# Kernel tuning notes

Hardware: AMD Instinct MI355X
Metric: run time of the kernel (lower is better)

Reference implementation:

```python
import jax, jax.numpy as jnp
import numpy as np

A = 32           # num_atoms
R = A * (A - 1)  # num_rel (fully connected, no self loops)
B, T, D = 4, 64, 64
S, E = 4, 4      # num_states, edge_types
MH, MO, NH = 256, 256, 256

def _lrelu(x):
    return jax.nn.leaky_relu(x, 0.01)  # torch default slope

def setup_inputs() -> dict:
    key = jax.random.key(0)
    ks = jax.random.split(key, 16)
    # one-hot receiver/sender matrices for a fully connected graph
    off = np.ones((A, A)) - np.eye(A)
    rec_idx, send_idx = np.where(off)
    eye = np.eye(A, dtype=np.float32)
    rel_rec = jnp.asarray(eye[rec_idx])    # [R, A]
    rel_send = jnp.asarray(eye[send_idx])  # [R, A]
    w = 0.05
    return {
        "inputs": jax.random.normal(ks[0], (B, A, T, D), jnp.float32),
        "state": jax.random.uniform(ks[1], (B, A, T, S), jnp.float32),
        "rel_type": jax.random.uniform(ks[2], (B, R, S, E), jnp.float32),
        "rel_rec": rel_rec,
        "rel_send": rel_send,
        "msg_fc1_w": jax.random.normal(ks[3], (E, 2 * D, MH), jnp.float32) * w,
        "msg_fc1_b": jax.random.normal(ks[4], (E, MH), jnp.float32) * w,
        "msg_fc2_w": jax.random.normal(ks[5], (E, MH, MO), jnp.float32) * w,
        "msg_fc2_b": jax.random.normal(ks[6], (E, MO), jnp.float32) * w,
        "out_fc1_w": jax.random.normal(ks[7], (D + MO, NH), jnp.float32) * w,
        "out_fc1_b": jax.random.normal(ks[8], (NH,), jnp.float32) * w,
        "out_fc2_w": jax.random.normal(ks[9], (NH, NH), jnp.float32) * w,
        "out_fc2_b": jax.random.normal(ks[10], (NH,), jnp.float32) * w,
        "out_fc3_w": jax.random.normal(ks[11], (NH, D), jnp.float32) * w,
        "out_fc3_b": jax.random.normal(ks[12], (D,), jnp.float32) * w,
        "pred_steps": 1,
    }

def reference(inputs, state, rel_type, rel_rec, rel_send,
              msg_fc1_w, msg_fc1_b, msg_fc2_w, msg_fc2_b,
              out_fc1_w, out_fc1_b, out_fc2_w, out_fc2_b,
              out_fc3_w, out_fc3_b, pred_steps):
    # hidden_states=True, embedding=False, ball_pos=None, skip_first=True,
    # dropout p=0, pred_steps=1 -> one single_step_forward over all T.
    x = jnp.transpose(inputs, (0, 2, 1, 3))   # [B,T,A,D]
    st = jnp.transpose(state, (0, 2, 1, 3))   # [B,T,A,S]
    t = x.shape[1]

    # gather via one-hot matmuls
    recv = jnp.einsum('ra,btad->btrd', rel_rec, x)    # [B,T,R,D]
    send = jnp.einsum('ra,btad->btrd', rel_send, x)   # [B,T,R,D]
    ss = jnp.einsum('ra,btas->btrs', rel_send, st)    # [B,T,R,S]
    pre_msg = jnp.concatenate([send, recv], axis=-1)  # [B,T,R,2D]

    all_msgs = jnp.zeros(pre_msg.shape[:3] + (MO,), pre_msg.dtype)
    for i in range(1, E):  # skip_first_edge_type
        m = _lrelu(pre_msg @ msg_fc1_w[i] + msg_fc1_b[i])
        m = _lrelu(m @ msg_fc2_w[i] + msg_fc2_b[i])
        # gate: sum over states of rel_type[...,i] * sender states
        g = jnp.einsum('brs,btrs->btr', rel_type[..., i], ss)[..., None]
        all_msgs = all_msgs + m * g

    # scatter-accumulate messages back to receiver nodes
    agg = jnp.einsum('btrm,ra->btam', all_msgs, rel_rec)  # [B,T,A,MO]
    aug = jnp.concatenate([x, agg], axis=-1)              # skip_connection = inputs
    h = _lrelu(aug @ out_fc1_w + out_fc1_b)
    h = _lrelu(h @ out_fc2_w + out_fc2_b)
    pred = h @ out_fc3_w + out_fc3_b
    nxt = x + pred                                        # [B,T,A,D]

    out = nxt[:, : t - 1]                                 # pred_all
    return jnp.transpose(out, (0, 2, 1, 3))               # [B,A,T-1,D]
```

## Files before the change

### kernel.cpp

```cpp
#include <hip/hip_runtime.h>


typedef _Float16 f16x8 __attribute__((ext_vector_type(8)));
typedef float f32x4 __attribute__((ext_vector_type(4)));

#define MFMAH(a, b, c) __builtin_amdgcn_mfma_f32_16x16x32_f16((a), (b), (c), 0, 0, 0)

#define KBAR0() do {                                             \
  __builtin_amdgcn_sched_barrier(0);                             \
  asm volatile("s_waitcnt vmcnt(0) lgkmcnt(0)" ::: "memory");    \
  __builtin_amdgcn_s_barrier();                                  \
  __builtin_amdgcn_sched_barrier(0);                             \
} while (0)

__device__ __forceinline__ unsigned pkh(float lo, float hi) {
  auto h = __builtin_amdgcn_cvt_pkrtz(lo, hi);
  return __builtin_bit_cast(unsigned, h);
}
__device__ __forceinline__ unsigned short f2h(float f) {
  return __builtin_bit_cast(unsigned short, (_Float16)f);
}
__device__ __forceinline__ float lrelu(float x) { return x > 0.f ? x : 0.01f * x; }

__device__ __forceinline__ void gl16(const void* g, void* l) {
  __builtin_amdgcn_global_load_lds(
      (const __attribute__((address_space(1))) unsigned int*)(unsigned long long)g,
      (__attribute__((address_space(3))) unsigned int*)(unsigned int)(unsigned long long)l,
      16, 0, 0);
}

__global__ __launch_bounds__(256) void kw(
    const float* __restrict__ w1, const float* __restrict__ w2,
    const float* __restrict__ o1, const float* __restrict__ o2, const float* __restrict__ o3,
    unsigned short* __restrict__ W1T, unsigned short* __restrict__ W2F,
    unsigned short* __restrict__ O1T, unsigned short* __restrict__ O2T,
    unsigned short* __restrict__ O3T) {
  int i = blockIdx.x * 256 + threadIdx.x;
  if (i < 98304) {
    int k = i & 63, n = (i >> 6) & 255, eh = i >> 14;
    int e = (eh >> 1) + 1, half = eh & 1;
    W1T[i] = f2h(w1[(e * 128 + half * 64 + k) * 256 + n]);
    return;
  }
  i -= 98304;
  if (i < 196608) {
    int j = i & 7, l = (i >> 3) & 63, t = (i >> 9) & 15, s = (i >> 13) & 7, e = i >> 16;
    int n = t * 16 + (l & 15);
    int k = s * 32 + (l >> 4) * 8 + j;
    W2F[i] = f2h(w2[(e + 1) * 65536 + k * 256 + n]);
    return;
  }
  i -= 196608;
  if (i < 81920) {
    int k = i % 320, n = i / 320;
    O1T[i] = f2h(o1[k * 256 + n]);
    return;
  }
  i -= 81920;
  if (i < 65536) {
    int k = i & 255, n = i >> 8;
    O2T[i] = f2h(o2[k * 256 + n]);
    return;
  }
  i -= 65536;
  {
    int k = i & 255, n = i >> 8;
    O3T[i] = f2h(o3[k * 64 + n]);
  }
}

__global__ __launch_bounds__(256) void ka(
    const float* __restrict__ inputs, const float* __restrict__ state,
    const float* __restrict__ rel_type, const unsigned short* __restrict__ W1T,
    const float* __restrict__ b1g,
    unsigned short* __restrict__ P, float* __restrict__ G) {
  int t = blockIdx.x, b = blockIdx.y;
  int bt = b * 63 + t;
  int tid = threadIdx.x, lane = tid & 63, wid = tid >> 6;
  int waveM = wid & 1, waveN = wid >> 1;
  __shared__ __align__(16) _Float16 xa[32 * 72];
  __shared__ __align__(16) _Float16 Bt[256 * 72];
  __shared__ __align__(16) _Float16 Ps[32 * 256];
  __shared__ float ss[32][4];
  {
    int a = tid >> 3, d0 = (tid & 7) * 8;
    const float* src = inputs + (((b * 32 + a) * 64 + t) << 6) + d0;
    float4 v0 = *(const float4*)src;
    float4 v1 = *(const float4*)(src + 4);
    uint4 w;
    w.x = pkh(v0.x, v0.y); w.y = pkh(v0.z, v0.w);
    w.z = pkh(v1.x, v1.y); w.w = pkh(v1.z, v1.w);
    *(uint4*)&xa[a * 72 + d0] = w;
  }
  if (tid < 128) {
    int a = tid >> 2, s = tid & 3;
    ss[a][s] = state[((b * 32 + a) * 64 + t) * 4 + s];
  }
  __syncthreads();
  #pragma unroll
  for (int q = 0; q < 12; ++q) {
    int task = tid + q * 256;
    int e = task >> 10, rem = task & 1023, a = rem >> 5, k = rem & 31;
    float g = 0.f;
    if (k < 31) {
      int sA = k + (k >= a ? 1 : 0);
      int r = a * 31 + k;
      const float* rt = rel_type + (b * 992 + r) * 16 + (e + 1);
      g = rt[0] * ss[sA][0] + rt[4] * ss[sA][1] + rt[8] * ss[sA][2] + rt[12] * ss[sA][3];
    }
    G[(bt * 3 + e) * 1024 + a * 32 + k] = g;
  }
  for (int eh = 0; eh < 6; ++eh) {
    #pragma unroll
    for (int q = 0; q < 8; ++q) {
      int cid = tid + q * 256;
      int n = cid >> 3, c8 = (cid & 7) * 8;
      *(uint4*)&Bt[n * 72 + c8] = *(const uint4*)&W1T[(eh * 256 + n) * 64 + c8];
    }
    __syncthreads();
    f32x4 acc[8];
    #pragma unroll
    for (int f = 0; f < 8; ++f) acc[f] = f32x4{0.f, 0.f, 0.f, 0.f};
    #pragma unroll
    for (int ik = 0; ik < 2; ++ik) {
      int k0 = ik * 32;
      f16x8 av = *(const f16x8*)&xa[(waveM * 16 + (lane & 15)) * 72 + k0 + (lane >> 4) * 8];
      #pragma unroll
      for (int f = 0; f < 8; ++f) {
        f16x8 bv = *(const f16x8*)&Bt[(waveN * 128 + f * 16 + (lane & 15)) * 72 + k0 + (lane >> 4) * 8];
        acc[f] = MFMAH(av, bv, acc[f]);
      }
    }
    #pragma unroll
    for (int f = 0; f < 8; ++f) {
      int c = waveN * 128 + f * 16 + (lane & 15);
      float bias = (eh & 1) ? b1g[((eh >> 1) + 1) * 256 + c] : 0.f;
      #pragma unroll
      for (int i = 0; i < 4; ++i) {
        int rrow = waveM * 16 + (lane >> 4) * 4 + i;
        Ps[rrow * 256 + c] = (_Float16)(acc[f][i] + bias);
      }
    }
    __syncthreads();
    unsigned short* dst = P + (bt * 6 + eh) * 8192;
    #pragma unroll
    for (int q = 0; q < 4; ++q) {
      int o = (tid + q * 256) * 8;
      *(uint4*)&dst[o] = *(const uint4*)&Ps[o];
    }
    __syncthreads();
  }
}

__global__ __launch_bounds__(512, 6) void kb(
    const unsigned short* __restrict__ P, const float* __restrict__ G,
    const unsigned short* __restrict__ W2F, const float* __restrict__ b2g,
    unsigned short* __restrict__ AGG3) {
  int bx = blockIdx.x;
  int swz = (bx & 7) * 1512 + (bx >> 3);
  int e = swz / 4032;
  int rem = swz - e * 4032;
  int bt = rem >> 4;
  int sub = rem & 15;
  int q = sub >> 1, nh = sub & 1;
  int a0 = q * 4;
  int tid = threadIdx.x, lane = tid & 63, wid = tid >> 6;
  int waveM = wid & 3, waveN = wid >> 2;
  int lane15 = lane & 15, kqh = lane >> 4;

  __shared__ __align__(16) _Float16 h1F[2][4096];
  __shared__ __align__(16) _Float16 Bt[3][4096];
  __shared__ float gs[128];
  __shared__ float b2s[128];

  const unsigned short* psrc  = P + (bt * 6 + e * 2) * 8192;
  const unsigned short* prsrc = psrc + 8192;
  const unsigned short* w2f = W2F + e * 65536 + nh * 8 * 512;

  int rrow = wid * 16 + lane15;
  int al0 = rrow >> 5, bk = rrow & 31;
  int bs = (bk < 31) ? bk + (bk >= a0 + al0 ? 1 : 0) : 0;
  const unsigned short* pvg = psrc + bs * 256 + kqh * 8;
  const unsigned short* rvg = prsrc + (a0 + al0) * 256 + kqh * 8;
  int h1off = wid * 512 + lane * 8;

  {
    f16x8 pv0 = *(const f16x8*)(pvg);
    f16x8 rv0 = *(const f16x8*)(rvg);
    __builtin_amdgcn_sched_barrier(0);
    gl16(w2f + tid * 8, (char*)&Bt[0][0] + tid * 16);
    gl16(w2f + 8192 + tid * 8, (char*)&Bt[1][0] + tid * 16);
    if (tid < 128) gs[tid] = G[((bt * 3 + e) << 10) + a0 * 32 + tid];
    else if (tid < 256) b2s[tid - 128] = b2g[(e + 1) * 256 + nh * 128 + (tid - 128)];
    f16x8 h = pv0 + rv0;
    *(f16x8*)&h1F[0][h1off] = __builtin_elementwise_max(h, h * (_Float16)0.01f);
  }
  KBAR0();

  f32x4 acc[2][4];
  #pragma unroll
  for (int f = 0; f < 2; ++f)
    #pragma unroll
    for (int g2 = 0; g2 < 4; ++g2) acc[f][g2] = f32x4{0.f, 0.f, 0.f, 0.f};

  #pragma unroll
  for (int s = 0; s < 8; ++s) {
    const int buf = s & 1;
    f16x8 pv, rv;
    if (s < 7) {
      pv = *(const f16x8*)(pvg + (s + 1) * 32);
      rv = *(const f16x8*)(rvg + (s + 1) * 32);
    }
    __builtin_amdgcn_sched_barrier(0);
    if (s < 6)
      gl16(w2f + (s + 2) * 8192 + tid * 8, (char*)&Bt[(s + 2) % 3][0] + tid * 16);
    __builtin_amdgcn_sched_barrier(0);
    f16x8 af0 = *(const f16x8*)&h1F[buf][(waveM * 2 + 0) * 512 + lane * 8];
    f16x8 af1 = *(const f16x8*)&h1F[buf][(waveM * 2 + 1) * 512 + lane * 8];
    __builtin_amdgcn_s_setprio(1);
    #pragma unroll
    for (int g2 = 0; g2 < 4; ++g2) {
      f16x8 bv = *(const f16x8*)&Bt[s % 3][(waveN * 4 + g2) * 512 + lane * 8];
      acc[0][g2] = MFMAH(af0, bv, acc[0][g2]);
      acc[1][g2] = MFMAH(af1, bv, acc[1][g2]);
    }
    __builtin_amdgcn_s_setprio(0);
    if (s < 7) {
      f16x8 h = pv + rv;
      *(f16x8*)&h1F[buf ^ 1][h1off] = __builtin_elementwise_max(h, h * (_Float16)0.01f);
      __builtin_amdgcn_sched_barrier(0);
      if (s < 6) asm volatile("s_waitcnt vmcnt(1)" ::: "memory");
      else       asm volatile("s_waitcnt vmcnt(0)" ::: "memory");
      asm volatile("s_waitcnt lgkmcnt(0)" ::: "memory");
      __builtin_amdgcn_s_barrier();
      __builtin_amdgcn_sched_barrier(0);
    }
  }

  _Float16* aggh = (_Float16*)AGG3;
  int al = a0 + waveM;
  #pragma unroll
  for (int g2 = 0; g2 < 4; ++g2) {
    int cl = (waveN * 4 + g2) * 16 + lane15;
    float bb = b2s[cl];
    float p = 0.f;
    #pragma unroll
    for (int f = 0; f < 2; ++f) {
      int k4 = f * 16 + kqh * 4;
      #pragma unroll
      for (int i = 0; i < 4; ++i)
        p += gs[waveM * 32 + k4 + i] * lrelu(acc[f][g2][i] + bb);
    }
    p += __shfl_xor(p, 16, 64);
    p += __shfl_xor(p, 32, 64);
    if (lane < 16)
      aggh[(size_t)e * 2064384 + (((bt * 32 + al) << 8) + nh * 128 + cl)] = (_Float16)p;
  }
}

__global__ __launch_bounds__(256) void kc(
    const float* __restrict__ inputs, const unsigned short* __restrict__ AGG3,
    const unsigned short* __restrict__ O1T, const unsigned short* __restrict__ O2T,
    const unsigned short* __restrict__ O3T,
    const float* __restrict__ ob1, const float* __restrict__ ob2, const float* __restrict__ ob3,
    float* __restrict__ out) {
  int t = blockIdx.x, b = blockIdx.y;
  int bt = b * 63 + t;
  int tid = threadIdx.x, lane = tid & 63, wid = tid >> 6;
  int waveM = wid & 1, waveN = wid >> 1;
  __shared__ __align__(16) _Float16 aug[32 * 328];
  __shared__ __align__(16) _Float16 h1[32 * 264];
  __shared__ __align__(16) _Float16 h2[32 * 264];
  __shared__ __align__(16) _Float16 Bt[256 * 40];
  __shared__ __align__(16) float xs[32 * 64];
  __shared__ float lb1[256], lb2[256], lb3[64];
  {
    int a = tid >> 3, d0 = (tid & 7) * 8;
    const float* src = inputs + (((b * 32 + a) * 64 + t) << 6) + d0;
    float4 v0 = *(const float4*)src;
    float4 v1 = *(const float4*)(src + 4);
    *(float4*)&xs[a * 64 + d0] = v0;
    *(float4*)&xs[a * 64 + d0 + 4] = v1;
    uint4 w;
    w.x = pkh(v0.x, v0.y); w.y = pkh(v0.z, v0.w);
    w.z = pkh(v1.x, v1.y); w.w = pkh(v1.z, v1.w);
    *(uint4*)&aug[a * 328 + d0] = w;
  }
  #pragma unroll
  for (int qq = 0; qq < 4; ++qq) {
    int cid = tid + qq * 256;
    int a = cid >> 5, c8 = (cid & 31) * 8;
    size_t o = ((size_t)(bt * 32 + a) << 8) + c8;
    f16x8 v0 = *(const f16x8*)&AGG3[o];
    f16x8 v1 = *(const f16x8*)&AGG3[2064384 + o];
    f16x8 v2 = *(const f16x8*)&AGG3[4128768 + o];
    f16x8 s = v0 + v1 + v2;
    *(uint4*)&aug[a * 328 + 64 + c8] = __builtin_bit_cast(uint4, s);
  }
  lb1[tid] = ob1[tid];
  lb2[tid] = ob2[tid];
  if (tid < 64) lb3[tid] = ob3[tid];
  __syncthreads();
  f32x4 acc[8];
  #pragma unroll
  for (int f = 0; f < 8; ++f) acc[f] = f32x4{0.f, 0.f, 0.f, 0.f};
  for (int kk = 0; kk < 10; ++kk) {
    #pragma unroll
    for (int q = 0; q < 4; ++q) {
      int cid = tid + q * 256;
      int n = cid >> 2, c8 = (cid & 3) * 8;
      *(uint4*)&Bt[n * 40 + c8] = *(const uint4*)&O1T[n * 320 + kk * 32 + c8];
    }
    __syncthreads();
    f16x8 av = *(const f16x8*)&aug[(waveM * 16 + (lane & 15)) * 328 + kk * 32 + (lane >> 4) * 8];
    #pragma unroll
    for (int f = 0; f < 8; ++f) {
      f16x8 bv = *(const f16x8*)&Bt[(waveN * 128 + f * 16 + (lane & 15)) * 40 + (lane >> 4) * 8];
      acc[f] = MFMAH(av, bv, acc[f]);
    }
    __syncthreads();
  }
  #pragma unroll
  for (int f = 0; f < 8; ++f) {
    int c = waveN * 128 + f * 16 + (lane & 15);
    #pragma unroll
    for (int i = 0; i < 4; ++i) {
      int r = waveM * 16 + (lane >> 4) * 4 + i;
      h1[r * 264 + c] = (_Float16)lrelu(acc[f][i] + lb1[c]);
    }
  }
  __syncthreads();
  #pragma unroll
  for (int f = 0; f < 8; ++f) acc[f] = f32x4{0.f, 0.f, 0.f, 0.f};
  for (int kk = 0; kk < 8; ++kk) {
    #pragma unroll
    for (int q = 0; q < 4; ++q) {
      int cid = tid + q * 256;
      int n = cid >> 2, c8 = (cid & 3) * 8;
      *(uint4*)&Bt[n * 40 + c8] = *(const uint4*)&O2T[n * 256 + kk * 32 + c8];
    }
    __syncthreads();
    f16x8 av = *(const f16x8*)&h1[(waveM * 16 + (lane & 15)) * 264 + kk * 32 + (lane >> 4) * 8];
    #pragma unroll
    for (int f = 0; f < 8; ++f) {
      f16x8 bv = *(const f16x8*)&Bt[(waveN * 128 + f * 16 + (lane & 15)) * 40 + (lane >> 4) * 8];
      acc[f] = MFMAH(av, bv, acc[f]);
    }
    __syncthreads();
  }
  #pragma unroll
  for (int f = 0; f < 8; ++f) {
    int c = waveN * 128 + f * 16 + (lane & 15);
    #pragma unroll
    for (int i = 0; i < 4; ++i) {
      int r = waveM * 16 + (lane >> 4) * 4 + i;
      h2[r * 264 + c] = (_Float16)lrelu(acc[f][i] + lb2[c]);
    }
  }
  __syncthreads();
  f32x4 a3[2];
  a3[0] = f32x4{0.f, 0.f, 0.f, 0.f};
  a3[1] = f32x4{0.f, 0.f, 0.f, 0.f};
  for (int kk = 0; kk < 8; ++kk) {
    {
      int n = tid >> 2, c8 = (tid & 3) * 8;
      *(uint4*)&Bt[n * 40 + c8] = *(const uint4*)&O3T[n * 256 + kk * 32 + c8];
    }
    __syncthreads();
    f16x8 av = *(const f16x8*)&h2[(waveM * 16 + (lane & 15)) * 264 + kk * 32 + (lane >> 4) * 8];
    #pragma unroll
    for (int f = 0; f < 2; ++f) {
      f16x8 bv = *(const f16x8*)&Bt[(waveN * 32 + f * 16 + (lane & 15)) * 40 + (lane >> 4) * 8];
      a3[f] = MFMAH(av, bv, a3[f]);
    }
    __syncthreads();
  }
  #pragma unroll
  for (int f = 0; f < 2; ++f) {
    int d = waveN * 32 + f * 16 + (lane & 15);
    #pragma unroll
    for (int i = 0; i < 4; ++i) {
      int a = waveM * 16 + (lane >> 4) * 4 + i;
      out[((b * 32 + a) * 63 + t) * 64 + d] = a3[f][i] + lb3[d] + xs[a * 64 + d];
    }
  }
}

extern "C" void kernel_launch(void* const* d_in, const int* in_sizes, int n_in,
                              void* d_out, int out_size, void* d_ws, size_t ws_size,
                              hipStream_t stream) {
  const float* inputs   = (const float*)d_in[0];
  const float* state    = (const float*)d_in[1];
  const float* rel_type = (const float*)d_in[2];
  const float* w1  = (const float*)d_in[5];
  const float* b1  = (const float*)d_in[6];
  const float* w2  = (const float*)d_in[7];
  const float* b2  = (const float*)d_in[8];
  const float* o1w = (const float*)d_in[9];
  const float* o1b = (const float*)d_in[10];
  const float* o2w = (const float*)d_in[11];
  const float* o2b = (const float*)d_in[12];
  const float* o3w = (const float*)d_in[13];
  const float* o3b = (const float*)d_in[14];
  char* ws = (char*)d_ws;
  unsigned short* W1T = (unsigned short*)(ws + 0);
  unsigned short* W2F = (unsigned short*)(ws + 196608);
  unsigned short* O1T = (unsigned short*)(ws + 589824);
  unsigned short* O2T = (unsigned short*)(ws + 753664);
  unsigned short* O3T = (unsigned short*)(ws + 884736);
  unsigned short* Pp  = (unsigned short*)(ws + 917504);
  float* G    = (float*)(ws + 25690112);
  unsigned short* AGG3 = (unsigned short*)(ws + 28786688);
  float* out = (float*)d_out;

  kw<<<1792, 256, 0, stream>>>(w1, w2, o1w, o2w, o3w, W1T, W2F, O1T, O2T, O3T);
  ka<<<dim3(63, 4), 256, 0, stream>>>(inputs, state, rel_type, W1T, b1, Pp, G);
  kb<<<12096, 512, 0, stream>>>(Pp, G, W2F, b2, AGG3);
  kc<<<dim3(63, 4), 256, 0, stream>>>(inputs, AGG3, O1T, O2T, O3T, o1b, o2b, o3b, out);
}
```

Measured before the change: 191.8 us.

## Preload whole weight slice into LDS and build A fragments in registers

Kernel kb now loads the entire 64KB W2 slice for its N-half into shared memory up front, instead of streaming it through a triple-buffered ring. Each wave builds its own A-operand fragments (leaky-relu of P+R) directly in registers rather than writing h1 to LDS and reading it back. This removes the per-step block barriers and LDS round trips. In exchange, LDS use grows from about 40KB to 64KB per block, so the occupancy hint drops from 6 to 4, which reduces latency hiding. All weight loads also now sit before the first compute.

Measured after the change: 269.0 us. 40.3% more time.

```diff
diff --git a/kernel.cpp b/kernel.cpp
--- a/kernel.cpp
+++ b/kernel.cpp
@@ -152,7 +152,7 @@
   }
 }
 
-__global__ __launch_bounds__(512, 6) void kb(
+__global__ __launch_bounds__(512, 4) void kb(
     const unsigned short* __restrict__ P, const float* __restrict__ G,
     const unsigned short* __restrict__ W2F, const float* __restrict__ b2g,
     unsigned short* __restrict__ AGG3) {
@@ -168,77 +168,78 @@
   int waveM = wid & 3, waveN = wid >> 2;
   int lane15 = lane & 15, kqh = lane >> 4;
 
-  __shared__ __align__(16) _Float16 h1F[2][4096];
-  __shared__ __align__(16) _Float16 Bt[3][4096];
+  __shared__ __align__(16) _Float16 Bp[32768];
   __shared__ float gs[128];
   __shared__ float b2s[128];
 
   const unsigned short* psrc  = P + (bt * 6 + e * 2) * 8192;
   const unsigned short* prsrc = psrc + 8192;
-  const unsigned short* w2f = W2F + e * 65536 + nh * 8 * 512;
-
-  int rrow = wid * 16 + lane15;
-  int al0 = rrow >> 5, bk = rrow & 31;
-  int bs = (bk < 31) ? bk + (bk >= a0 + al0 ? 1 : 0) : 0;
-  const unsigned short* pvg = psrc + bs * 256 + kqh * 8;
-  const unsigned short* rvg = prsrc + (a0 + al0) * 256 + kqh * 8;
-  int h1off = wid * 512 + lane * 8;
-
+  const unsigned short* w2f   = W2F + e * 65536 + nh * 4096;
+
+  int al = a0 + waveM;
+  int bk0 = lane15;
+  int bk1 = 16 + lane15;
+  int bs0 = bk0 + (bk0 >= al ? 1 : 0);
+  int bs1 = (bk1 < 31) ? (bk1 + (bk1 >= al ? 1 : 0)) : 0;
+  const unsigned short* pv0g = psrc + bs0 * 256 + kqh * 8;
+  const unsigned short* pv1g = psrc + bs1 * 256 + kqh * 8;
+  const unsigned short* rvg  = prsrc + al * 256 + kqh * 8;
+
+  f16x8 pvA = *(const f16x8*)pv0g;
+  f16x8 pvB = *(const f16x8*)pv1g;
+  f16x8 rv0 = *(const f16x8*)rvg;
+  __builtin_amdgcn_sched_barrier(0);
+  #pragma unroll
+  for (int j = 0; j < 8; ++j) {
+    int c = j * 512 + tid;
+    gl16(w2f + (c >> 9) * 8192 + (c & 511) * 8, (char*)&Bp[0] + c * 16);
+  }
+  if (tid < 128) gs[tid] = G[((bt * 3 + e) << 10) + a0 * 32 + tid];
+  else if (tid < 256) b2s[tid - 128] = b2g[(e + 1) * 256 + nh * 128 + (tid - 128)];
+  f16x8 af0, af1;
   {
-    f16x8 pv0 = *(const f16x8*)(pvg);
-    f16x8 rv0 = *(const f16x8*)(rvg);
+    f16x8 h = pvA + rv0;
+    af0 = __builtin_elementwise_max(h, h * (_Float16)0.01f);
+    h = pvB + rv0;
+    af1 = __builtin_elementwise_max(h, h * (_Float16)0.01f);
+  }
+  KBAR0();
+
+  f32x4 acc[2][4];
+  #pragma unroll
+  for (int f = 0; f < 2; ++f)
+    #pragma unroll
+    for (int g2 = 0; g2 < 4; ++g2) acc[f][g2] = f32x4{0.f, 0.f, 0.f, 0.f};
+
+  #pragma unroll
+  for (int s = 0; s < 8; ++s) {
+    f16x8 pA, pB, rN;
+    if (s < 7) {
+      pA = *(const f16x8*)(pv0g + (s + 1) * 32);
+      pB = *(const f16x8*)(pv1g + (s + 1) * 32);
+      rN = *(const f16x8*)(rvg + (s + 1) * 32);
+    }
     __builtin_amdgcn_sched_barrier(0);
-    gl16(w2f + tid * 8, (char*)&Bt[0][0] + tid * 16);
-    gl16(w2f + 8192 + tid * 8, (char*)&Bt[1][0] + tid * 16);
-    if (tid < 128) gs[tid] = G[((bt * 3 + e) << 10) + a0 * 32 + tid];
-    else if (tid < 256) b2s[tid - 128] = b2g[(e + 1) * 256 + nh * 128 + (tid - 128)];
-    f16x8 h = pv0 + rv0;
-    *(f16x8*)&h1F[0][h1off] = __builtin_elementwise_max(h, h * (_Float16)0.01f);
-  }
-  KBAR0();
-
-  f32x4 acc[2][4];
-  #pragma unroll
-  for (int f = 0; f < 2; ++f)
-    #pragma unroll
-    for (int g2 = 0; g2 < 4; ++g2) acc[f][g2] = f32x4{0.f, 0.f, 0.f, 0.f};
-
-  #pragma unroll
-  for (int s = 0; s < 8; ++s) {
-    const int buf = s & 1;
-    f16x8 pv, rv;
-    if (s < 7) {
-      pv = *(const f16x8*)(pvg + (s + 1) * 32);
-      rv = *(const f16x8*)(rvg + (s + 1) * 32);
-    }
-    __builtin_amdgcn_sched_barrier(0);
-    if (s < 6)
-      gl16(w2f + (s + 2) * 8192 + tid * 8, (char*)&Bt[(s + 2) % 3][0] + tid * 16);
-    __builtin_amdgcn_sched_barrier(0);
-    f16x8 af0 = *(const f16x8*)&h1F[buf][(waveM * 2 + 0) * 512 + lane * 8];
-    f16x8 af1 = *(const f16x8*)&h1F[buf][(waveM * 2 + 1) * 512 + lane * 8];
+    f16x8 bv[4];
+    #pragma unroll
+    for (int g2 = 0; g2 < 4; ++g2)
+      bv[g2] = *(const f16x8*)&Bp[s * 4096 + (waveN * 4 + g2) * 512 + lane * 8];
     __builtin_amdgcn_s_setprio(1);
     #pragma unroll
     for (int g2 = 0; g2 < 4; ++g2) {
-      f16x8 bv = *(const f16x8*)&Bt[s % 3][(waveN * 4 + g2) * 512 + lane * 8];
-      acc[0][g2] = MFMAH(af0, bv, acc[0][g2]);
-      acc[1][g2] = MFMAH(af1, bv, acc[1][g2]);
+      acc[0][g2] = MFMAH(af0, bv[g2], acc[0][g2]);
+      acc[1][g2] = MFMAH(af1, bv[g2], acc[1][g2]);
     }
     __builtin_amdgcn_s_setprio(0);
     if (s < 7) {
-      f16x8 h = pv + rv;
-      *(f16x8*)&h1F[buf ^ 1][h1off] = __builtin_elementwise_max(h, h * (_Float16)0.01f);
-      __builtin_amdgcn_sched_barrier(0);
-      if (s < 6) asm volatile("s_waitcnt vmcnt(1)" ::: "memory");
-      else       asm volatile("s_waitcnt vmcnt(0)" ::: "memory");
-      asm volatile("s_waitcnt lgkmcnt(0)" ::: "memory");
-      __builtin_amdgcn_s_barrier();
-      __builtin_amdgcn_sched_barrier(0);
+      f16x8 h = pA + rN;
+      af0 = __builtin_elementwise_max(h, h * (_Float16)0.01f);
+      h = pB + rN;
+      af1 = __builtin_elementwise_max(h, h * (_Float16)0.01f);
     }
   }
 
   _Float16* aggh = (_Float16*)AGG3;
-  int al = a0 + waveM;
   #pragma unroll
   for (int g2 = 0; g2 < 4; ++g2) {
     int cl = (waveN * 4 + g2) * 16 + lane15;
```
